# Kernel optimization log

Measured on AMD Instinct MI355X. Metric: run time of the kernel, lower is better.

## Reference

```python
import jax, jax.numpy as jnp
import numpy as np

VOCAB = 128
NUM_PATHS = 100     # num_paths sampled from the lattice
NBEST_SCALE = 0.5   # scale on scores before sampling (k2.random_paths)
TEMPERATURE = 1.0   # logprob temperature before normalization
BLANK = 0           # CTC blank token


def setup_inputs() -> dict:
    key = jax.random.key(0)
    k1, k2, k3, k4 = jax.random.split(key, 4)
    B, T, L = 8, 500, 100
    logits = jax.random.normal(k1, (B, T, VOCAB), jnp.float32)
    emissions = jax.nn.log_softmax(logits, -1)  # acoustic-model log-probs (N, T, C)
    emissions_lengths = jax.random.randint(k2, (B,), 400, T + 1).astype(jnp.int32)
    labels = jax.random.randint(k3, (B, L), 1, VOCAB).astype(jnp.int32)
    labels_length = jax.random.randint(k4, (B,), 80, L + 1).astype(jnp.int32)
    return {"emissions": emissions, "emissions_lengths": emissions_lengths,
            "labels": labels, "labels_length": labels_length}


def _mwer(emissions, emissions_lengths, labels, labels_length):
    B, T, V = emissions.shape
    L = labels.shape[1]
    P = NUM_PATHS
    key = jax.random.key(1)
    # --- N-best path sampling: Gumbel perturbation of nbest_scale-scaled log-probs ---
    u = jax.random.uniform(key, (B, P, T, V), emissions.dtype, 1e-6, 1.0 - 1e-6)
    g = -jnp.log(-jnp.log(u))
    tokens = jnp.argmax(emissions[:, None] * NBEST_SCALE + g, axis=-1)  # (B, P, T)
    frame_mask = jnp.arange(T)[None, None, :] < emissions_lengths[:, None, None]
    # path log-prob under the model (unscaled scores), temperature-scaled
    lp = jnp.take_along_axis(emissions[:, None], tokens[..., None], axis=-1)[..., 0]
    path_logp = jnp.sum(jnp.where(frame_mask, lp, 0.0), axis=-1) / TEMPERATURE  # (B, P)
    # --- CTC collapse (ctc_topo semantics: drop blanks + repeats) into padded hyps ---
    prev = jnp.concatenate([jnp.full_like(tokens[..., :1], -1), tokens[..., :-1]], -1)
    keep = (tokens != BLANK) & (tokens != prev) & frame_mask
    pos = jnp.where(keep, jnp.cumsum(keep, -1) - 1, T)  # dropped frames -> dump slot T
    BP = B * P
    tok2, pos2 = tokens.reshape(BP, T), pos.reshape(BP, T)
    hyp = jnp.full((BP, T + 1), -1, tokens.dtype).at[jnp.arange(BP)[:, None], pos2].set(tok2)[:, :T]
    hyp_len = keep.reshape(BP, T).sum(-1)
    # --- Levenshtein alignment: exact edit distance hyp vs ref (vectorized DP) ---
    refs = jnp.repeat(labels, P, axis=0)             # (BP, L)  hyp_to_ref_map
    ref_len = jnp.repeat(labels_length, P, axis=0)   # (BP,)
    dp0 = jnp.broadcast_to(jnp.arange(L + 1, dtype=jnp.int32), (BP, L + 1))
    js = jnp.arange(L + 1, dtype=jnp.int32)[None, :]

    def step(dp, x):
        h, valid = x  # hyp token (BP,), valid flag (BP,)
        cost = (refs != h[:, None]).astype(jnp.int32)                       # (BP, L)
        cand = jnp.concatenate([dp[:, :1] + 1,
                                jnp.minimum(dp[:, 1:] + 1, dp[:, :-1] + cost)], 1)
        # insertion chain new[j] = min(cand[j], new[j-1]+1) via min-plus prefix
        new = jax.lax.cummin(cand - js, axis=1) + js
        return jnp.where(valid[:, None], new, dp), None

    valid = jnp.arange(T)[:, None] < hyp_len[None, :]  # (T, BP)
    dp, _ = jax.lax.scan(step, dp0, (hyp.T, valid))
    wers = jnp.take_along_axis(dp, ref_len[:, None], 1)[:, 0].reshape(B, P)
    wers = jax.lax.stop_gradient(wers.astype(emissions.dtype))
    # --- MWER: normalize path posteriors per utterance, expected WER, 'mean' ---
    prob = jax.nn.softmax(path_logp, axis=1)
    return jnp.mean(prob * wers)


def reference(emissions, emissions_lengths, labels, labels_length):
    return _mwer(emissions, emissions_lengths, labels, labels_length)
```

## Files before the change

### kernel.cpp

```cpp
#include <hip/hip_runtime.h>
#include <stdint.h>

#define NB 8
#define NP 100
#define NT 500
#define NV 128
#define NBP 800
#define TS 512
#define NITEMS (NB * NT * 50)

typedef unsigned long long u64;

#define ROTL(x, r) __builtin_amdgcn_alignbit((x), (x), 32 - (r))

__device__ __forceinline__ uint32_t threefry01_lo(uint32_t x0, uint32_t x1) {
  const uint32_t k0 = 0u, k1 = 1u;
  const uint32_t k2 = 0x1BD11BDAu ^ k0 ^ k1;
  x0 += k0; x1 += k1;
#define TF_R(r) { x0 += x1; x1 = ROTL(x1, r); x1 ^= x0; }
  TF_R(13) TF_R(15) TF_R(26) TF_R(6)
  x0 += k1; x1 += k2 + 1u;
  TF_R(17) TF_R(29) TF_R(16) TF_R(24)
  x0 += k2; x1 += k0 + 2u;
  TF_R(13) TF_R(15) TF_R(26) TF_R(6)
  x0 += k0; x1 += k1 + 3u;
  TF_R(17) TF_R(29) TF_R(16) TF_R(24)
  x0 += k1; x1 += k2 + 4u;
  TF_R(13) TF_R(15) TF_R(26) TF_R(6)
  x1 += k0 + 5u;
#undef TF_R
  return x1;
}

__global__ __launch_bounds__(256) void k_sample(
    const float* __restrict__ em, const int* __restrict__ elen,
    uint8_t* __restrict__ tok2, float* __restrict__ lp2t, int item_base) {
  __shared__ float snw[3][NV + 1];
  const int tid = threadIdx.x;
  const int i0 = item_base + blockIdx.x * 64;
  const int R0 = i0 / 50;
  for (int i = tid; i < 3 * NV; i += 256) {
    const int r = i >> 7, v = i & 127;
    int R = R0 + r; R = R < NB * NT ? R : NB * NT - 1;
    snw[r][v] = -__builtin_amdgcn_exp2f(em[(size_t)R * NV + v] * -0.7213475204444817f);
  }
  __syncthreads();
  const int item = i0 + (tid >> 2);
  const int q = tid & 3;
  if (item >= NITEMS) return;
  const int R = item / 50;
  const int pp = item - R * 50;
  const int b = R / NT;
  const int t = R - b * NT;
  if (t >= elen[b]) return;
  const int r = R - R0;
  const int vh = q << 5;
  const int bp0 = b * NP + 2 * pp;
  const uint32_t base0 = ((uint32_t)(bp0 * NT + t) << 7) + (uint32_t)vh;
  const uint32_t base1 = base0 + (uint32_t)(NT << 7);
  const float span = (float)(1.0 - 1e-6) - 1e-6f;
  float best0 = 3.0e38f, best1 = 3.0e38f;
  int bi0 = 0, bi1 = 0;
#pragma unroll 8
  for (int i = 0; i < 32; i++) {
    const uint32_t r0 = threefry01_lo(0u, base0 + (uint32_t)i);
    const uint32_t r1 = threefry01_lo(0u, base1 + (uint32_t)i);
    const float f0 = __uint_as_float((r0 >> 9) | 0x3f800000u) - 1.0f;
    const float f1 = __uint_as_float((r1 >> 9) | 0x3f800000u) - 1.0f;
    const float u0 = fmaf(f0, span, 1e-6f);
    const float u1 = fmaf(f1, span, 1e-6f);
    const float w = snw[r][vh + i];
    const float s0 = __log2f(u0) * w;
    const float s1 = __log2f(u1) * w;
    if (s0 < best0) { best0 = s0; bi0 = vh + i; }
    if (s1 < best1) { best1 = s1; bi1 = vh + i; }
  }
#pragma unroll
  for (int off = 1; off <= 2; off <<= 1) {
    const float oa = __shfl_xor(best0, off); const int ia = __shfl_xor(bi0, off);
    if (oa < best0 || (oa == best0 && ia < bi0)) { best0 = oa; bi0 = ia; }
    const float ob = __shfl_xor(best1, off); const int ib = __shfl_xor(bi1, off);
    if (ob < best1 || (ob == best1 && ib < bi1)) { best1 = ob; bi1 = ib; }
  }
  if (q == 0) {
    const float e0 = em[(size_t)R * NV + bi0];
    const float e1 = em[(size_t)R * NV + bi1];
    tok2[(size_t)bp0 * TS + t] = (uint8_t)bi0;
    tok2[(size_t)(bp0 + 1) * TS + t] = (uint8_t)bi1;
    *(float2*)&lp2t[(size_t)t * NBP + bp0] = make_float2(e0, e1);
  }
}

__global__ __launch_bounds__(256) void k_eq(
    const uint8_t* __restrict__ tok2, const int* __restrict__ labels,
    const int* __restrict__ llen, const int* __restrict__ elen,
    uint4* __restrict__ eqt) {
  __shared__ uint32_t pq[4][NV];
  const int b = blockIdx.x;
  const int pg = blockIdx.y;
  const int tid = threadIdx.x;
  const int m = llen[b];
  if (tid < NV) {
    const int c = tid;
    const int* __restrict__ lab = labels + b * 100;
    uint32_t a0 = 0, a1 = 0, a2 = 0, a3 = 0;
    const int e0 = m < 32 ? m : 32, e1 = m < 64 ? m : 64;
    const int e2 = m < 96 ? m : 96, e3 = m;
    for (int i = 0; i < e0; i++)  a0 |= (uint32_t)(lab[i] == c) << i;
    for (int i = 32; i < e1; i++) a1 |= (uint32_t)(lab[i] == c) << (i - 32);
    for (int i = 64; i < e2; i++) a2 |= (uint32_t)(lab[i] == c) << (i - 64);
    for (int i = 96; i < e3; i++) a3 |= (uint32_t)(lab[i] == c) << (i - 96);
    pq[0][c] = a0; pq[1][c] = a1; pq[2][c] = a2; pq[3][c] = a3;
  }
  __syncthreads();
  const int el = elen[b];
  const int bp0 = b * NP + pg * 4;
  const uint8_t* __restrict__ src = tok2 + (size_t)bp0 * TS;
  for (int f = tid; f < 4 * NT; f += 256) {
    const int pl = f & 3, t = f >> 2;
    if (t >= el) break;
    const int c = src[(size_t)pl * TS + t];
    uint4 E;
    E.x = pq[0][c]; E.y = pq[1][c];
    E.z = pq[2][c]; E.w = pq[3][c] | ((uint32_t)c << 24);
    eqt[(size_t)t * NBP + bp0 + pl] = E;
  }
}

__device__ __forceinline__ void loadg(uint4 (&B)[4], int g, int bp,
                                      const uint4* __restrict__ eqt) {
#pragma unroll
  for (int i = 0; i < 4; i++) {
    int t = g * 4 + i;
    t = t < NT ? t : NT - 1;
    B[i] = eqt[(size_t)t * NBP + bp];
  }
}

__device__ __forceinline__ void procg(const uint4 (&B)[4], int g, int myel,
                                      u64 hmask,
                                      u64& Pv0, u64& Pv1, u64& Mv0, u64& Mv1,
                                      int& score, int& prev) {
#pragma unroll
  for (int i = 0; i < 4; i++) {
    if (g * 4 + i >= myel) break;
    const int c = B[i].w >> 24;
    const u64 Eq0 = (u64)B[i].x | ((u64)B[i].y << 32);
    const u64 Eq1 = (u64)B[i].z | ((u64)(B[i].w & 0x00FFFFFFu) << 32);
    const bool kept = (c != 0) & (c != prev);
    prev = c;
    const u64 Xv0 = Eq0 | Mv0, Xv1 = Eq1 | Mv1;
    const u64 EP0 = Eq0 & Pv0, EP1 = Eq1 & Pv1;
    const u64 sA = EP0 + Pv0;
    const u64 sB = EP1 + Pv1 + (sA < EP0 ? 1ull : 0ull);
    const u64 Xh0 = (sA ^ Pv0) | Eq0;
    const u64 Xh1 = (sB ^ Pv1) | Eq1;
    const u64 Ph0 = Mv0 | ~(Xh0 | Pv0);
    const u64 Ph1 = Mv1 | ~(Xh1 | Pv1);
    const u64 Mh0 = Pv0 & Xh0, Mh1 = Pv1 & Xh1;
    const int d = (int)((Ph1 & hmask) != 0) - (int)((Mh1 & hmask) != 0);
    const u64 nPh1 = (Ph1 << 1) | (Ph0 >> 63);
    const u64 nPh0 = (Ph0 << 1) | 1ull;
    const u64 nMh1 = (Mh1 << 1) | (Mh0 >> 63);
    const u64 nMh0 = (Mh0 << 1);
    score += kept ? d : 0;
    Pv0 = kept ? (nMh0 | ~(Xv0 | nPh0)) : Pv0;
    Pv1 = kept ? (nMh1 | ~(Xv1 | nPh1)) : Pv1;
    Mv0 = kept ? (nPh0 & Xv0) : Mv0;
    Mv1 = kept ? (nPh1 & Xv1) : Mv1;
  }
}

__global__ __launch_bounds__(64) void k_dp(
    const uint4* __restrict__ eqt,
    const int* __restrict__ elen, const int* __restrict__ llen,
    float* __restrict__ wer) {
  const int b = blockIdx.x, h = blockIdx.y;
  const int tid = threadIdx.x;
  const bool active = (tid < 50);
  const int bp = b * NP + h * 50 + (active ? tid : 49);
  const int m = llen[b];
  const int myel = elen[b];
  u64 Pv0 = ~0ull, Pv1 = ~0ull, Mv0 = 0ull, Mv1 = 0ull;
  int score = m, prev = -1;
  const u64 hmask = 1ull << ((m - 1) & 63);

  const int ng = (myel + 3) >> 2;
  uint4 B0[4], B1[4], B2[4], B3[4];
  loadg(B0, 0, bp, eqt); loadg(B1, 1, bp, eqt);
  loadg(B2, 2, bp, eqt); loadg(B3, 3, bp, eqt);
  int g = 0;
  while (g + 4 <= ng) {
    procg(B0, g,     myel, hmask, Pv0, Pv1, Mv0, Mv1, score, prev);
    loadg(B0, g + 4, bp, eqt);
    procg(B1, g + 1, myel, hmask, Pv0, Pv1, Mv0, Mv1, score, prev);
    loadg(B1, g + 5, bp, eqt);
    procg(B2, g + 2, myel, hmask, Pv0, Pv1, Mv0, Mv1, score, prev);
    loadg(B2, g + 6, bp, eqt);
    procg(B3, g + 3, myel, hmask, Pv0, Pv1, Mv0, Mv1, score, prev);
    loadg(B3, g + 7, bp, eqt);
    g += 4;
  }
  if (g     < ng) procg(B0, g,     myel, hmask, Pv0, Pv1, Mv0, Mv1, score, prev);
  if (g + 1 < ng) procg(B1, g + 1, myel, hmask, Pv0, Pv1, Mv0, Mv1, score, prev);
  if (g + 2 < ng) procg(B2, g + 2, myel, hmask, Pv0, Pv1, Mv0, Mv1, score, prev);
  if (active) wer[bp] = (float)score;
}

__global__ __launch_bounds__(128) void k_red(
    const float* __restrict__ lp2t, const int* __restrict__ elen,
    double* __restrict__ pred) {
  const int b = blockIdx.x, k = blockIdx.y;
  const int tid = threadIdx.x;
  const bool active = (tid < NP);
  const int p = active ? tid : NP - 1;
  const int el = elen[b];
  const int t0 = k * 125;
  const int t1 = (t0 + 125 < el) ? t0 + 125 : el;
  const float* __restrict__ col = lp2t + b * NP + p;
  double s = 0.0;
#pragma unroll 8
  for (int t = t0; t < t1; t++) s += (double)col[(size_t)t * NBP];
  if (active) pred[(size_t)(b * NP + p) * 4 + k] = s;
}

__global__ __launch_bounds__(512) void k_fin(
    const double* __restrict__ pred, const float* __restrict__ wer,
    float* __restrict__ out) {
  __shared__ float partial[NB];
  const int w = threadIdx.x >> 6, lane = threadIdx.x & 63;
  const int base = w * NP;
  float l0 = -1e30f, l1 = -1e30f;
  if (lane < NP) {
    const double* pr = pred + (size_t)(base + lane) * 4;
    l0 = (float)(pr[0] + pr[1] + pr[2] + pr[3]);
  }
  if (lane + 64 < NP) {
    const double* pr = pred + (size_t)(base + lane + 64) * 4;
    l1 = (float)(pr[0] + pr[1] + pr[2] + pr[3]);
  }
  float mx = fmaxf(l0, l1);
  for (int off = 1; off < 64; off <<= 1) mx = fmaxf(mx, __shfl_xor(mx, off));
  const float e0 = (lane < NP) ? __expf(l0 - mx) : 0.0f;
  const float e1 = (lane + 64 < NP) ? __expf(l1 - mx) : 0.0f;
  const float w0 = (lane < NP) ? wer[base + lane] : 0.0f;
  const float w1 = (lane + 64 < NP) ? wer[base + lane + 64] : 0.0f;
  float s = e0 + e1;
  float a = e0 * w0 + e1 * w1;
  for (int off = 1; off < 64; off <<= 1) {
    s += __shfl_xor(s, off);
    a += __shfl_xor(a, off);
  }
  if (lane == 0) partial[w] = a / s;
  __syncthreads();
  if (threadIdx.x == 0) {
    float tot = 0.0f;
    for (int i = 0; i < NB; i++) tot += partial[i];
    out[0] = tot * (1.0f / (float)NBP);
  }
}

extern "C" void kernel_launch(void* const* d_in, const int* in_sizes, int n_in,
                              void* d_out, int out_size, void* d_ws, size_t ws_size,
                              hipStream_t stream) {
  const float* em     = (const float*)d_in[0];
  const int*   elen   = (const int*)d_in[1];
  const int*   labels = (const int*)d_in[2];
  const int*   llen   = (const int*)d_in[3];
  float* out = (float*)d_out;
  char* ws = (char*)d_ws;
  uint4*   eqt  = (uint4*)ws;
  uint8_t* tok2 = (uint8_t*)(ws + 6400000);
  float*   lp2t = (float*)(ws + 6400000 + 409600);
  float*   wer  = (float*)(ws + 6400000 + 409600 + 1600000);
  double*  pred = (double*)(ws + 6400000 + 409600 + 1600000 + 3200);
  float*   slpX = (float*)(ws + 6400000 + 409600 + 1600000 + 3200 + 25600);
  (void)slpX; (void)ws_size;

  k_sample<<<dim3(1563), dim3(256), 0, stream>>>(em, elen, tok2, lp2t, 0);
  k_sample<<<dim3(1562), dim3(256), 0, stream>>>(em, elen, tok2, lp2t, 1563 * 64);
  k_eq<<<dim3(NB, 25), dim3(256), 0, stream>>>(tok2, labels, llen, elen, eqt);
  k_dp<<<dim3(NB, 2), dim3(64), 0, stream>>>(eqt, elen, llen, wer);
  k_red<<<dim3(NB, 4), dim3(128), 0, stream>>>(lp2t, elen, pred);
  k_fin<<<dim3(1), dim3(512), 0, stream>>>(pred, wer, out);
}
```

Baseline: 208.2 us.

## Compact kept CTC tokens before bit-parallel edit-distance DP

Splits the match-mask building into a per-utterance label bitmask kernel and a per-path compaction kernel. The compaction kernel uses a wave ballot and mbcnt to write only non-blank, non-repeat frames into a per-path row and records how many were kept. The serial Myers DP then loops only over the kept symbols and drops the per-step kept selects, which shortens its critical path. The cost is an extra kernel launch and a path-major layout, so DP loads are strided per lane instead of coalesced across paths.

```diff
diff --git a/kernel.cpp b/kernel.cpp
--- a/kernel.cpp
+++ b/kernel.cpp
@@ -7,6 +7,7 @@
 #define NV 128
 #define NBP 800
 #define TS 512
+#define ES 500
 #define NITEMS (NB * NT * 50)
 
 typedef unsigned long long u64;
@@ -91,64 +92,72 @@
   }
 }
 
-__global__ __launch_bounds__(256) void k_eq(
-    const uint8_t* __restrict__ tok2, const int* __restrict__ labels,
-    const int* __restrict__ llen, const int* __restrict__ elen,
-    uint4* __restrict__ eqt) {
-  __shared__ uint32_t pq[4][NV];
+__global__ __launch_bounds__(128) void k_pq(
+    const int* __restrict__ labels, const int* __restrict__ llen,
+    uint4* __restrict__ pqg) {
   const int b = blockIdx.x;
-  const int pg = blockIdx.y;
-  const int tid = threadIdx.x;
+  const int c = threadIdx.x;
   const int m = llen[b];
-  if (tid < NV) {
-    const int c = tid;
-    const int* __restrict__ lab = labels + b * 100;
-    uint32_t a0 = 0, a1 = 0, a2 = 0, a3 = 0;
-    const int e0 = m < 32 ? m : 32, e1 = m < 64 ? m : 64;
-    const int e2 = m < 96 ? m : 96, e3 = m;
-    for (int i = 0; i < e0; i++)  a0 |= (uint32_t)(lab[i] == c) << i;
-    for (int i = 32; i < e1; i++) a1 |= (uint32_t)(lab[i] == c) << (i - 32);
-    for (int i = 64; i < e2; i++) a2 |= (uint32_t)(lab[i] == c) << (i - 64);
-    for (int i = 96; i < e3; i++) a3 |= (uint32_t)(lab[i] == c) << (i - 96);
-    pq[0][c] = a0; pq[1][c] = a1; pq[2][c] = a2; pq[3][c] = a3;
-  }
+  const int* __restrict__ lab = labels + b * 100;
+  uint32_t a0 = 0, a1 = 0, a2 = 0, a3 = 0;
+  const int e0 = m < 32 ? m : 32, e1 = m < 64 ? m : 64;
+  const int e2 = m < 96 ? m : 96, e3 = m;
+  for (int i = 0; i < e0; i++)  a0 |= (uint32_t)(lab[i] == c) << i;
+  for (int i = 32; i < e1; i++) a1 |= (uint32_t)(lab[i] == c) << (i - 32);
+  for (int i = 64; i < e2; i++) a2 |= (uint32_t)(lab[i] == c) << (i - 64);
+  for (int i = 96; i < e3; i++) a3 |= (uint32_t)(lab[i] == c) << (i - 96);
+  pqg[b * NV + c] = make_uint4(a0, a1, a2, a3);
+}
+
+__global__ __launch_bounds__(64) void k_ce(
+    const uint8_t* __restrict__ tok2, const uint4* __restrict__ pqg,
+    const int* __restrict__ elen, uint4* __restrict__ eqc,
+    int* __restrict__ nkept) {
+  __shared__ uint4 pqs[NV];
+  const int bp = blockIdx.x;
+  const int b = bp / NP;
+  const int lane = threadIdx.x;
+  pqs[lane] = pqg[b * NV + lane];
+  pqs[lane + 64] = pqg[b * NV + lane + 64];
   __syncthreads();
   const int el = elen[b];
-  const int bp0 = b * NP + pg * 4;
-  const uint8_t* __restrict__ src = tok2 + (size_t)bp0 * TS;
-  for (int f = tid; f < 4 * NT; f += 256) {
-    const int pl = f & 3, t = f >> 2;
-    if (t >= el) break;
-    const int c = src[(size_t)pl * TS + t];
-    uint4 E;
-    E.x = pq[0][c]; E.y = pq[1][c];
-    E.z = pq[2][c]; E.w = pq[3][c] | ((uint32_t)c << 24);
-    eqt[(size_t)t * NBP + bp0 + pl] = E;
-  }
-}
-
-__device__ __forceinline__ void loadg(uint4 (&B)[4], int g, int bp,
-                                      const uint4* __restrict__ eqt) {
+  const uint8_t* __restrict__ row = tok2 + (size_t)bp * TS;
+  uint4* __restrict__ orow = eqc + (size_t)bp * ES;
+  int off = 0;
+  for (int t0 = 0; t0 < el; t0 += 64) {
+    const int t = t0 + lane;
+    const bool inb = (t < el);
+    const int c = inb ? row[t] : 0;
+    const int cp = (t == 0) ? 255 : (inb ? row[t - 1] : 255);
+    const bool kept = inb && (c != 0) && (c != cp);
+    const u64 mask = __ballot(kept);
+    const int idx = off + (int)__builtin_amdgcn_mbcnt_hi(
+        (uint32_t)(mask >> 32),
+        __builtin_amdgcn_mbcnt_lo((uint32_t)mask, 0u));
+    if (kept) orow[idx] = pqs[c];
+    off += (int)__popcll(mask);
+  }
+  if (lane == 0) nkept[bp] = off;
+}
+
+__device__ __forceinline__ void loadg(uint4 (&B)[4], int g, const uint4* __restrict__ rowp) {
 #pragma unroll
   for (int i = 0; i < 4; i++) {
     int t = g * 4 + i;
-    t = t < NT ? t : NT - 1;
-    B[i] = eqt[(size_t)t * NBP + bp];
-  }
-}
-
-__device__ __forceinline__ void procg(const uint4 (&B)[4], int g, int myel,
+    t = t < ES ? t : ES - 1;
+    B[i] = rowp[t];
+  }
+}
+
+__device__ __forceinline__ void procg(const uint4 (&B)[4], int fbase, int nk,
                                       u64 hmask,
                                       u64& Pv0, u64& Pv1, u64& Mv0, u64& Mv1,
-                                      int& score, int& prev) {
+                                      int& score) {
 #pragma unroll
   for (int i = 0; i < 4; i++) {
-    if (g * 4 + i >= myel) break;
-    const int c = B[i].w >> 24;
+    if (fbase + i >= nk) break;
     const u64 Eq0 = (u64)B[i].x | ((u64)B[i].y << 32);
-    const u64 Eq1 = (u64)B[i].z | ((u64)(B[i].w & 0x00FFFFFFu) << 32);
-    const bool kept = (c != 0) & (c != prev);
-    prev = c;
+    const u64 Eq1 = (u64)B[i].z | ((u64)B[i].w << 32);
     const u64 Xv0 = Eq0 | Mv0, Xv1 = Eq1 | Mv1;
     const u64 EP0 = Eq0 & Pv0, EP1 = Eq1 & Pv1;
     const u64 sA = EP0 + Pv0;
@@ -158,52 +167,56 @@
     const u64 Ph0 = Mv0 | ~(Xh0 | Pv0);
     const u64 Ph1 = Mv1 | ~(Xh1 | Pv1);
     const u64 Mh0 = Pv0 & Xh0, Mh1 = Pv1 & Xh1;
-    const int d = (int)((Ph1 & hmask) != 0) - (int)((Mh1 & hmask) != 0);
+    score += (int)((Ph1 & hmask) != 0) - (int)((Mh1 & hmask) != 0);
     const u64 nPh1 = (Ph1 << 1) | (Ph0 >> 63);
     const u64 nPh0 = (Ph0 << 1) | 1ull;
     const u64 nMh1 = (Mh1 << 1) | (Mh0 >> 63);
     const u64 nMh0 = (Mh0 << 1);
-    score += kept ? d : 0;
-    Pv0 = kept ? (nMh0 | ~(Xv0 | nPh0)) : Pv0;
-    Pv1 = kept ? (nMh1 | ~(Xv1 | nPh1)) : Pv1;
-    Mv0 = kept ? (nPh0 & Xv0) : Mv0;
-    Mv1 = kept ? (nPh1 & Xv1) : Mv1;
+    Pv0 = nMh0 | ~(Xv0 | nPh0);
+    Pv1 = nMh1 | ~(Xv1 | nPh1);
+    Mv0 = nPh0 & Xv0;
+    Mv1 = nPh1 & Xv1;
   }
 }
 
 __global__ __launch_bounds__(64) void k_dp(
-    const uint4* __restrict__ eqt,
-    const int* __restrict__ elen, const int* __restrict__ llen,
-    float* __restrict__ wer) {
+    const uint4* __restrict__ eqc, const int* __restrict__ nkept,
+    const int* __restrict__ llen, float* __restrict__ wer) {
   const int b = blockIdx.x, h = blockIdx.y;
   const int tid = threadIdx.x;
   const bool active = (tid < 50);
   const int bp = b * NP + h * 50 + (active ? tid : 49);
   const int m = llen[b];
-  const int myel = elen[b];
+  const int nk = nkept[bp];
+  const uint4* __restrict__ rowp = eqc + (size_t)bp * ES;
   u64 Pv0 = ~0ull, Pv1 = ~0ull, Mv0 = 0ull, Mv1 = 0ull;
-  int score = m, prev = -1;
+  int score = m;
   const u64 hmask = 1ull << ((m - 1) & 63);
 
-  const int ng = (myel + 3) >> 2;
+  const int ngl = (nk + 3) >> 2;
+  int ngmax = ngl;
+  for (int off = 1; off < 64; off <<= 1) {
+    const int o = __shfl_xor(ngmax, off);
+    ngmax = o > ngmax ? o : ngmax;
+  }
   uint4 B0[4], B1[4], B2[4], B3[4];
-  loadg(B0, 0, bp, eqt); loadg(B1, 1, bp, eqt);
-  loadg(B2, 2, bp, eqt); loadg(B3, 3, bp, eqt);
+  loadg(B0, 0, rowp); loadg(B1, 1, rowp);
+  loadg(B2, 2, rowp); loadg(B3, 3, rowp);
   int g = 0;
-  while (g + 4 <= ng) {
-    procg(B0, g,     myel, hmask, Pv0, Pv1, Mv0, Mv1, score, prev);
-    loadg(B0, g + 4, bp, eqt);
-    procg(B1, g + 1, myel, hmask, Pv0, Pv1, Mv0, Mv1, score, prev);
-    loadg(B1, g + 5, bp, eqt);
-    procg(B2, g + 2, myel, hmask, Pv0, Pv1, Mv0, Mv1, score, prev);
-    loadg(B2, g + 6, bp, eqt);
-    procg(B3, g + 3, myel, hmask, Pv0, Pv1, Mv0, Mv1, score, prev);
-    loadg(B3, g + 7, bp, eqt);
+  while (g + 4 <= ngmax) {
+    procg(B0, (g    ) * 4, nk, hmask, Pv0, Pv1, Mv0, Mv1, score);
+    loadg(B0, g + 4, rowp);
+    procg(B1, (g + 1) * 4, nk, hmask, Pv0, Pv1, Mv0, Mv1, score);
+    loadg(B1, g + 5, rowp);
+    procg(B2, (g + 2) * 4, nk, hmask, Pv0, Pv1, Mv0, Mv1, score);
+    loadg(B2, g + 6, rowp);
+    procg(B3, (g + 3) * 4, nk, hmask, Pv0, Pv1, Mv0, Mv1, score);
+    loadg(B3, g + 7, rowp);
     g += 4;
   }
-  if (g     < ng) procg(B0, g,     myel, hmask, Pv0, Pv1, Mv0, Mv1, score, prev);
-  if (g + 1 < ng) procg(B1, g + 1, myel, hmask, Pv0, Pv1, Mv0, Mv1, score, prev);
-  if (g + 2 < ng) procg(B2, g + 2, myel, hmask, Pv0, Pv1, Mv0, Mv1, score, prev);
+  if (g     < ngmax) procg(B0, (g    ) * 4, nk, hmask, Pv0, Pv1, Mv0, Mv1, score);
+  if (g + 1 < ngmax) procg(B1, (g + 1) * 4, nk, hmask, Pv0, Pv1, Mv0, Mv1, score);
+  if (g + 2 < ngmax) procg(B2, (g + 2) * 4, nk, hmask, Pv0, Pv1, Mv0, Mv1, score);
   if (active) wer[bp] = (float)score;
 }
 
@@ -269,18 +282,19 @@
   const int*   llen   = (const int*)d_in[3];
   float* out = (float*)d_out;
   char* ws = (char*)d_ws;
-  uint4*   eqt  = (uint4*)ws;
-  uint8_t* tok2 = (uint8_t*)(ws + 6400000);
-  float*   lp2t = (float*)(ws + 6400000 + 409600);
-  float*   wer  = (float*)(ws + 6400000 + 409600 + 1600000);
-  double*  pred = (double*)(ws + 6400000 + 409600 + 1600000 + 3200);
-  float*   slpX = (float*)(ws + 6400000 + 409600 + 1600000 + 3200 + 25600);
-  (void)slpX; (void)ws_size;
+  uint4*   eqc   = (uint4*)ws;
+  uint8_t* tok2  = (uint8_t*)(ws + 6400000);
+  float*   lp2t  = (float*)(ws + 6809600);
+  float*   wer   = (float*)(ws + 8409600);
+  double*  pred  = (double*)(ws + 8412800);
+  int*     nkept = (int*)(ws + 8438400);
+  uint4*   pqg   = (uint4*)(ws + 8441600);
 
   k_sample<<<dim3(1563), dim3(256), 0, stream>>>(em, elen, tok2, lp2t, 0);
   k_sample<<<dim3(1562), dim3(256), 0, stream>>>(em, elen, tok2, lp2t, 1563 * 64);
-  k_eq<<<dim3(NB, 25), dim3(256), 0, stream>>>(tok2, labels, llen, elen, eqt);
-  k_dp<<<dim3(NB, 2), dim3(64), 0, stream>>>(eqt, elen, llen, wer);
+  k_pq<<<dim3(NB), dim3(128), 0, stream>>>(labels, llen, pqg);
+  k_ce<<<dim3(NBP), dim3(64), 0, stream>>>(tok2, pqg, elen, eqc, nkept);
+  k_dp<<<dim3(NB, 2), dim3(64), 0, stream>>>(eqc, nkept, llen, wer);
   k_red<<<dim3(NB, 4), dim3(128), 0, stream>>>(lp2t, elen, pred);
   k_fin<<<dim3(1), dim3(512), 0, stream>>>(pred, wer, out);
 }
```

Result: faster. 199.6 us (-4.1%).
